# Performance work log

Hardware: AMD Instinct MI355X
Metric: run time of the kernel (lower is better)

## Reference

```python
import jax, jax.numpy as jnp
import numpy as np

N_NODES = 100000
N_EDGES = 3200000  # avg degree 32
D_IN = 256
D_OUT = 256


def setup_inputs() -> dict:
    key = jax.random.key(0)
    k1, k2, k3, k4 = jax.random.split(key, 4)
    x = jax.random.normal(k1, (N_NODES, D_IN), dtype=jnp.float32)
    # nn.Linear(in, out, bias=False): weight shape [out, in]
    W = jax.random.normal(k2, (D_OUT, D_IN), dtype=jnp.float32) / np.sqrt(D_IN).astype(np.float32)
    bias = jnp.zeros((D_OUT,), dtype=jnp.float32)
    rows = jax.random.randint(k3, (N_EDGES,), 0, N_NODES, dtype=jnp.int32)
    cols = jax.random.randint(k4, (N_EDGES,), 0, N_NODES, dtype=jnp.int32)
    return {"x": x, "W": W, "bias": bias, "rows": rows, "cols": cols}


def reference(x, W, bias, rows, cols):
    # aggr == 'planetoid-gcn-residual' branch; dropout p=0 (identity).
    n = x.shape[0]
    h = x @ W.T + bias                                      # [N, D_out]
    # adj_t.sum(dim=-1): per-row degree of binary adjacency
    deg = jax.ops.segment_sum(jnp.ones(rows.shape, x.dtype), rows, num_segments=n)
    norm = jax.lax.rsqrt(1.0 + deg)[:, None]                # [N, 1]
    h = norm * h
    # spmm_add(adj_t, h)[i] = sum_{(i,j) in E} h[j]
    agg = jax.ops.segment_sum(h[cols], rows, num_segments=n)
    h = agg + h
    return norm * h
```

## Files before the change

kernel.cpp:

```cpp
#include <hip/hip_runtime.h>
#include <hip/hip_fp16.h>
#include <stdint.h>


#define THREADS 256
#define MAXBUCK 800
#define B3_EDGES 16384

typedef _Float16 half8 __attribute__((ext_vector_type(8)));
typedef float floatx4 __attribute__((ext_vector_type(4)));

__global__ __launch_bounds__(THREADS) void bucket_count(
    const int* __restrict__ rows, int* __restrict__ bcnt, int E, int nbuck) {
    __shared__ int h[MAXBUCK];
    for (int b = threadIdx.x; b < nbuck; b += THREADS) h[b] = 0;
    __syncthreads();
    int nquad  = E >> 2;
    int stride = gridDim.x * THREADS;
    for (int q = blockIdx.x * THREADS + threadIdx.x; q < nquad; q += stride) {
        int4 r = ((const int4*)rows)[q];
        atomicAdd(&h[r.x >> 7], 1);
        atomicAdd(&h[r.y >> 7], 1);
        atomicAdd(&h[r.z >> 7], 1);
        atomicAdd(&h[r.w >> 7], 1);
    }
    if (blockIdx.x == 0)
        for (int e = (nquad << 2) + threadIdx.x; e < E; e += THREADS)
            atomicAdd(&h[rows[e] >> 7], 1);
    __syncthreads();
    for (int b = threadIdx.x; b < nbuck; b += THREADS) {
        int v = h[b];
        if (v) atomicAdd(&bcnt[b], v);
    }
}

__global__ __launch_bounds__(THREADS) void bucket_scan(
    const int* __restrict__ bcnt, int* __restrict__ boff, int* __restrict__ bcur,
    int nbuck, int E) {
    __shared__ int s[THREADS];
    int tid = threadIdx.x;
    int i0  = tid * 4;
    int v0 = (i0 + 0 < nbuck) ? bcnt[i0 + 0] : 0;
    int v1 = (i0 + 1 < nbuck) ? bcnt[i0 + 1] : 0;
    int v2 = (i0 + 2 < nbuck) ? bcnt[i0 + 2] : 0;
    int v3 = (i0 + 3 < nbuck) ? bcnt[i0 + 3] : 0;
    int sum = v0 + v1 + v2 + v3;
    s[tid] = sum;
    __syncthreads();
    for (int off = 1; off < THREADS; off <<= 1) {
        int t = (tid >= off) ? s[tid - off] : 0;
        __syncthreads();
        s[tid] += t;
        __syncthreads();
    }
    int run = s[tid] - sum;
    if (i0 + 0 < nbuck) { boff[i0 + 0] = run; bcur[i0 + 0] = run; }  run += v0;
    if (i0 + 1 < nbuck) { boff[i0 + 1] = run; bcur[i0 + 1] = run; }  run += v1;
    if (i0 + 2 < nbuck) { boff[i0 + 2] = run; bcur[i0 + 2] = run; }  run += v2;
    if (i0 + 3 < nbuck) { boff[i0 + 3] = run; bcur[i0 + 3] = run; }
    if (tid == 0) boff[nbuck] = E;
}

__global__ __launch_bounds__(THREADS) void bucket_scatter(
    const int* __restrict__ rows, const int* __restrict__ cols,
    int* __restrict__ bcur, int2* __restrict__ buf, int E, int nbuck) {
    __shared__ int h[MAXBUCK];
    __shared__ int lbase[MAXBUCK];
    for (int b = threadIdx.x; b < nbuck; b += THREADS) h[b] = 0;
    __syncthreads();
    int e0 = blockIdx.x * B3_EDGES;
    int e1 = e0 + B3_EDGES; if (e1 > E) e1 = E;
    for (int e = e0 + threadIdx.x; e < e1; e += THREADS)
        atomicAdd(&h[rows[e] >> 7], 1);
    __syncthreads();
    for (int b = threadIdx.x; b < nbuck; b += THREADS) {
        int v = h[b];
        lbase[b] = v ? atomicAdd(&bcur[b], v) : 0;
        h[b] = 0;
    }
    __syncthreads();
    for (int e = e0 + threadIdx.x; e < e1; e += THREADS) {
        int r = rows[e];
        int c = cols[e];
        int b = r >> 7;
        int p = lbase[b] + atomicAdd(&h[b], 1);
        buf[p] = make_int2(r, c);
    }
}

__global__ __launch_bounds__(THREADS) void csr_finalize(
    const int2* __restrict__ buf, const int* __restrict__ boff,
    int* __restrict__ rs, int* __restrict__ csr, int n, int E) {
    int b = blockIdx.x;
    __shared__ int h[128];
    __shared__ int base[128];
    if (threadIdx.x < 128) h[threadIdx.x] = 0;
    __syncthreads();
    int s = boff[b], e = boff[b + 1];
    for (int i = s + threadIdx.x; i < e; i += THREADS)
        atomicAdd(&h[buf[i].x & 127], 1);
    __syncthreads();
    if (threadIdx.x < 128) base[threadIdx.x] = h[threadIdx.x];
    __syncthreads();
    for (int off = 1; off < 128; off <<= 1) {
        int t = 0;
        if (threadIdx.x < 128 && threadIdx.x >= off) t = base[threadIdx.x - off];
        __syncthreads();
        if (threadIdx.x < 128) base[threadIdx.x] += t;
        __syncthreads();
    }
    if (threadIdx.x < 128) {
        int excl = s + base[threadIdx.x] - h[threadIdx.x];
        base[threadIdx.x] = excl;
        int row = (b << 7) + threadIdx.x;
        if (row < n) rs[row] = excl;
        h[threadIdx.x] = 0;
    }
    if (b == 0 && threadIdx.x == 0) rs[n] = E;
    __syncthreads();
    for (int i = s + threadIdx.x; i < e; i += THREADS) {
        int2 rc = buf[i];
        int rl = rc.x & 127;
        int p = base[rl] + atomicAdd(&h[rl], 1);
        csr[p] = rc.y;
    }
}

__global__ void make_bswz(const float* __restrict__ W, half8* __restrict__ Bswz) {
    int t = blockIdx.x * THREADS + threadIdx.x;
    int n_tile = t >> 9;
    int k_step = (t >> 6) & 7;
    int lane   = t & 63;
    int q = lane >> 4, m16 = lane & 15;
    const float* src = W + (size_t)(n_tile * 16 + m16) * 256 + k_step * 32 + q * 8;
    half8 h;
#pragma unroll
    for (int j = 0; j < 8; j++) h[j] = (_Float16)src[j];
    Bswz[t] = h;
}

__device__ __forceinline__ int As_swz(int b) {
    return b ^ ((((b >> 10) & 7) ^ (((b >> 8) & 1) << 3)) << 4);
}

__global__ __launch_bounds__(THREADS) void gemm_mfma(
    const float* __restrict__ x, const half8* __restrict__ Bswz,
    const float* __restrict__ bias, const int* __restrict__ rs,
    _Float16* __restrict__ h16, int n) {
    __shared__ _Float16 As[4 * 8 * 64 * 8];
    int tid  = threadIdx.x;
    int row0 = blockIdx.x * 64;

#pragma unroll
    for (int i = 0; i < 16; i++) {
        int flat = i * THREADS + tid;
        int r  = flat >> 6;
        int k  = (flat & 63) * 4;
        float4 v;
        if (row0 + r < n) v = *(const float4*)(x + (size_t)(row0 + r) * 256 + k);
        else { v.x = 0.f; v.y = 0.f; v.z = 0.f; v.w = 0.f; }
        int m_sub  = r >> 4;
        int k_step = k >> 5;
        int q      = (k >> 3) & 3;
        int j      = k & 7;
        int lane_w = (r & 15) + (q << 4);
        int entry  = (m_sub * 8 + k_step) * 64 + lane_w;
        union { _Float16 h[4]; uint2 u; } pk;
        pk.h[0] = (_Float16)v.x; pk.h[1] = (_Float16)v.y;
        pk.h[2] = (_Float16)v.z; pk.h[3] = (_Float16)v.w;
        *(uint2*)((char*)As + As_swz(entry * 16 + (j << 1))) = pk.u;
    }
    __syncthreads();

    int w    = tid >> 6;
    int lane = tid & 63;

    floatx4 acc[4][4];
#pragma unroll
    for (int ms = 0; ms < 4; ms++)
#pragma unroll
        for (int nn = 0; nn < 4; nn++) {
            acc[ms][nn][0] = 0.f; acc[ms][nn][1] = 0.f;
            acc[ms][nn][2] = 0.f; acc[ms][nn][3] = 0.f;
        }

    for (int ks = 0; ks < 8; ks++) {
        half8 bfrag[4];
#pragma unroll
        for (int nn = 0; nn < 4; nn++)
            bfrag[nn] = Bswz[((w * 4 + nn) * 8 + ks) * 64 + lane];
        half8 afrag[4];
#pragma unroll
        for (int ms = 0; ms < 4; ms++)
            afrag[ms] = *(const half8*)((char*)As +
                            As_swz(((ms * 8 + ks) * 64 + lane) * 16));
#pragma unroll
        for (int ms = 0; ms < 4; ms++)
#pragma unroll
            for (int nn = 0; nn < 4; nn++)
                acc[ms][nn] = __builtin_amdgcn_mfma_f32_16x16x32_f16(
                    afrag[ms], bfrag[nn], acc[ms][nn], 0, 0, 0);
    }

    int rgrp = lane >> 4;
    int cl   = lane & 15;
#pragma unroll
    for (int ms = 0; ms < 4; ms++) {
        int rbase = row0 + ms * 16 + rgrp * 4;
        float nrm[4];
#pragma unroll
        for (int i = 0; i < 4; i++) {
            int r = rbase + i;
            nrm[i] = (r < n) ? rsqrtf(1.0f + (float)(rs[r + 1] - rs[r])) : 0.f;
        }
#pragma unroll
        for (int nn = 0; nn < 4; nn++) {
            int col = w * 64 + nn * 16 + cl;
            float bb = bias[col];
#pragma unroll
            for (int i = 0; i < 4; i++) {
                int r = rbase + i;
                if (r < n)
                    h16[(size_t)r * 256 + col] =
                        (_Float16)((acc[ms][nn][i] + bb) * nrm[i]);
            }
        }
    }
}

__global__ __launch_bounds__(THREADS) void agg_half(
    const _Float16* __restrict__ h16, const int* __restrict__ csr_col,
    const int* __restrict__ rs, float* __restrict__ out, int n, int halfsel) {
    int row = blockIdx.x * 4 + (threadIdx.x >> 6);
    if (row >= n) return;
    int lane = threadIdx.x & 63;
    int g    = lane >> 4;
    int l16  = lane & 15;
    int off  = halfsel * 128 + l16 * 8;
    const _Float16* hb = h16 + off;

    int s   = rs[row];
    int end = rs[row + 1];

    float acc[8] = {0.f, 0.f, 0.f, 0.f, 0.f, 0.f, 0.f, 0.f};
    if (g == 0) {
        half8 v = *(const half8*)(hb + (size_t)row * 256);
#pragma unroll
        for (int j = 0; j < 8; j++) acc[j] = (float)v[j];
    }

    int e = s + g;
    for (; e + 4 < end; e += 8) {
        int c0 = csr_col[e];
        int c1 = csr_col[e + 4];
        half8 v0 = *(const half8*)(hb + (size_t)c0 * 256);
        half8 v1 = *(const half8*)(hb + (size_t)c1 * 256);
#pragma unroll
        for (int j = 0; j < 8; j++) acc[j] += (float)v0[j] + (float)v1[j];
    }
    for (; e < end; e += 4) {
        int c = csr_col[e];
        half8 v = *(const half8*)(hb + (size_t)c * 256);
#pragma unroll
        for (int j = 0; j < 8; j++) acc[j] += (float)v[j];
    }

#pragma unroll
    for (int j = 0; j < 8; j++) acc[j] += __shfl_down(acc[j], 32);
#pragma unroll
    for (int j = 0; j < 8; j++) acc[j] += __shfl_down(acc[j], 16);

    if (g == 0) {
        float nrm = rsqrtf(1.0f + (float)(end - s));
        float4 o0, o1;
        o0.x = acc[0] * nrm; o0.y = acc[1] * nrm; o0.z = acc[2] * nrm; o0.w = acc[3] * nrm;
        o1.x = acc[4] * nrm; o1.y = acc[5] * nrm; o1.z = acc[6] * nrm; o1.w = acc[7] * nrm;
        float* dst = out + (size_t)row * 256 + off;
        *(float4*)dst       = o0;
        *(float4*)(dst + 4) = o1;
    }
}

extern "C" void kernel_launch(void* const* d_in, const int* in_sizes, int n_in,
                              void* d_out, int out_size, void* d_ws, size_t ws_size,
                              hipStream_t stream) {
    const float* x    = (const float*)d_in[0];
    const float* W    = (const float*)d_in[1];
    const float* bias = (const float*)d_in[2];
    const int*   rows = (const int*)d_in[3];
    const int*   cols = (const int*)d_in[4];

    const int D = 256;
    int n = in_sizes[0] / D;
    int E = in_sizes[3];
    int nbuck = (n + 127) >> 7;

    char* p = (char*)d_ws;
    auto alignup = [](size_t v) { return (v + 255) & ~(size_t)255; };
    _Float16* h16 = (_Float16*)p; p += alignup((size_t)n * D * sizeof(_Float16));
    int*   rs     = (int*)p;    p += alignup((size_t)(n + 1) * sizeof(int));
    int*   csr    = (int*)p;    p += alignup((size_t)E * sizeof(int));
    half8* Bswz   = (half8*)p;  p += alignup((size_t)8192 * sizeof(half8));
    int*   bcnt   = (int*)p;    p += alignup((size_t)MAXBUCK * sizeof(int));
    int*   boff   = (int*)p;    p += alignup((size_t)(MAXBUCK + 1) * sizeof(int));
    int*   bcur   = (int*)p;    p += alignup((size_t)MAXBUCK * sizeof(int));

    int2* buf = (int2*)h16;

    hipMemsetAsync(bcnt, 0, (size_t)nbuck * sizeof(int), stream);

    bucket_count<<<256, THREADS, 0, stream>>>(rows, bcnt, E, nbuck);
    bucket_scan<<<1, THREADS, 0, stream>>>(bcnt, boff, bcur, nbuck, E);

    int b3blocks = (E + B3_EDGES - 1) / B3_EDGES;
    bucket_scatter<<<b3blocks, THREADS, 0, stream>>>(rows, cols, bcur, buf, E, nbuck);

    csr_finalize<<<nbuck, THREADS, 0, stream>>>(buf, boff, rs, csr, n, E);

    make_bswz<<<32, THREADS, 0, stream>>>(W, Bswz);

    int gblocks = (n + 63) / 64;
    gemm_mfma<<<gblocks, THREADS, 0, stream>>>(x, Bswz, bias, rs, h16, n);

    int ablocks = (n + 3) / 4;
    agg_half<<<ablocks, THREADS, 0, stream>>>(h16, csr, rs, (float*)d_out, n, 0);
    agg_half<<<ablocks, THREADS, 0, stream>>>(h16, csr, rs, (float*)d_out, n, 1);
}
```

Baseline: 570.8 us.

## Use 512-row buckets with packed 32-bit edges and LDS-staged coalesced scatter

Buckets now cover 512 rows (196 buckets) instead of 128 rows (782). Each edge is packed into one 32-bit word (local row in the high bits, column in the low 17 bits), which halves the intermediate buffer traffic. The scatter kernel sorts each edge chunk by bucket in LDS and then writes each bucket's run contiguously, so global stores are coalesced rather than scattered. The final aggregation output uses nontemporal stores. The 17-bit column packing and the 256-bucket cap limit the node count this path can handle.

After: 548.8 us. 3.9% less time.

```diff
diff --git a/kernel.cpp b/kernel.cpp
--- a/kernel.cpp
+++ b/kernel.cpp
@@ -4,34 +4,32 @@
 
 
 #define THREADS 256
-#define MAXBUCK 800
-#define B3_EDGES 16384
+#define NB 256
+#define B3_EDGES 8192
 
 typedef _Float16 half8 __attribute__((ext_vector_type(8)));
 typedef float floatx4 __attribute__((ext_vector_type(4)));
 
 __global__ __launch_bounds__(THREADS) void bucket_count(
     const int* __restrict__ rows, int* __restrict__ bcnt, int E, int nbuck) {
-    __shared__ int h[MAXBUCK];
-    for (int b = threadIdx.x; b < nbuck; b += THREADS) h[b] = 0;
+    __shared__ int h[NB];
+    h[threadIdx.x] = 0;
     __syncthreads();
     int nquad  = E >> 2;
     int stride = gridDim.x * THREADS;
     for (int q = blockIdx.x * THREADS + threadIdx.x; q < nquad; q += stride) {
         int4 r = ((const int4*)rows)[q];
-        atomicAdd(&h[r.x >> 7], 1);
-        atomicAdd(&h[r.y >> 7], 1);
-        atomicAdd(&h[r.z >> 7], 1);
-        atomicAdd(&h[r.w >> 7], 1);
+        atomicAdd(&h[r.x >> 9], 1);
+        atomicAdd(&h[r.y >> 9], 1);
+        atomicAdd(&h[r.z >> 9], 1);
+        atomicAdd(&h[r.w >> 9], 1);
     }
     if (blockIdx.x == 0)
         for (int e = (nquad << 2) + threadIdx.x; e < E; e += THREADS)
-            atomicAdd(&h[rows[e] >> 7], 1);
-    __syncthreads();
-    for (int b = threadIdx.x; b < nbuck; b += THREADS) {
-        int v = h[b];
-        if (v) atomicAdd(&bcnt[b], v);
-    }
+            atomicAdd(&h[rows[e] >> 9], 1);
+    __syncthreads();
+    int v = h[threadIdx.x];
+    if (threadIdx.x < nbuck && v) atomicAdd(&bcnt[threadIdx.x], v);
 }
 
 __global__ __launch_bounds__(THREADS) void bucket_scan(
@@ -39,13 +37,8 @@
     int nbuck, int E) {
     __shared__ int s[THREADS];
     int tid = threadIdx.x;
-    int i0  = tid * 4;
-    int v0 = (i0 + 0 < nbuck) ? bcnt[i0 + 0] : 0;
-    int v1 = (i0 + 1 < nbuck) ? bcnt[i0 + 1] : 0;
-    int v2 = (i0 + 2 < nbuck) ? bcnt[i0 + 2] : 0;
-    int v3 = (i0 + 3 < nbuck) ? bcnt[i0 + 3] : 0;
-    int sum = v0 + v1 + v2 + v3;
-    s[tid] = sum;
+    int v = (tid < nbuck) ? bcnt[tid] : 0;
+    s[tid] = v;
     __syncthreads();
     for (int off = 1; off < THREADS; off <<= 1) {
         int t = (tid >= off) ? s[tid - off] : 0;
@@ -53,76 +46,94 @@
         s[tid] += t;
         __syncthreads();
     }
-    int run = s[tid] - sum;
-    if (i0 + 0 < nbuck) { boff[i0 + 0] = run; bcur[i0 + 0] = run; }  run += v0;
-    if (i0 + 1 < nbuck) { boff[i0 + 1] = run; bcur[i0 + 1] = run; }  run += v1;
-    if (i0 + 2 < nbuck) { boff[i0 + 2] = run; bcur[i0 + 2] = run; }  run += v2;
-    if (i0 + 3 < nbuck) { boff[i0 + 3] = run; bcur[i0 + 3] = run; }
+    int excl = s[tid] - v;
+    if (tid < nbuck) { boff[tid] = excl; bcur[tid] = excl; }
     if (tid == 0) boff[nbuck] = E;
 }
 
 __global__ __launch_bounds__(THREADS) void bucket_scatter(
     const int* __restrict__ rows, const int* __restrict__ cols,
-    int* __restrict__ bcur, int2* __restrict__ buf, int E, int nbuck) {
-    __shared__ int h[MAXBUCK];
-    __shared__ int lbase[MAXBUCK];
-    for (int b = threadIdx.x; b < nbuck; b += THREADS) h[b] = 0;
+    int* __restrict__ bcur, uint32_t* __restrict__ buf, int E, int nbuck) {
+    __shared__ uint32_t staged[B3_EDGES];
+    __shared__ int h[NB], lo[NB], gb[NB], hc[NB];
+    int tid = threadIdx.x;
+    h[tid] = 0; hc[tid] = 0;
     __syncthreads();
     int e0 = blockIdx.x * B3_EDGES;
     int e1 = e0 + B3_EDGES; if (e1 > E) e1 = E;
-    for (int e = e0 + threadIdx.x; e < e1; e += THREADS)
-        atomicAdd(&h[rows[e] >> 7], 1);
-    __syncthreads();
-    for (int b = threadIdx.x; b < nbuck; b += THREADS) {
-        int v = h[b];
-        lbase[b] = v ? atomicAdd(&bcur[b], v) : 0;
-        h[b] = 0;
-    }
-    __syncthreads();
-    for (int e = e0 + threadIdx.x; e < e1; e += THREADS) {
+    for (int e = e0 + tid; e < e1; e += THREADS)
+        atomicAdd(&h[rows[e] >> 9], 1);
+    __syncthreads();
+    int v = h[tid];
+    lo[tid] = v;
+    __syncthreads();
+    for (int off = 1; off < NB; off <<= 1) {
+        int t = (tid >= off) ? lo[tid - off] : 0;
+        __syncthreads();
+        lo[tid] += t;
+        __syncthreads();
+    }
+    int excl = lo[tid] - v;
+    __syncthreads();
+    lo[tid] = excl;
+    gb[tid] = (tid < nbuck && v) ? atomicAdd(&bcur[tid], v) : 0;
+    __syncthreads();
+    for (int e = e0 + tid; e < e1; e += THREADS) {
         int r = rows[e];
         int c = cols[e];
-        int b = r >> 7;
-        int p = lbase[b] + atomicAdd(&h[b], 1);
-        buf[p] = make_int2(r, c);
+        int b = r >> 9;
+        int p = lo[b] + atomicAdd(&hc[b], 1);
+        staged[p] = ((uint32_t)(r & 511) << 17) | (uint32_t)c;
+    }
+    __syncthreads();
+    int wid = tid >> 6, lane = tid & 63;
+    for (int b = wid; b < nbuck; b += 4) {
+        int cnt = h[b], src = lo[b], dst = gb[b];
+        for (int i = lane; i < cnt; i += 64)
+            buf[dst + i] = staged[src + i];
     }
 }
 
 __global__ __launch_bounds__(THREADS) void csr_finalize(
-    const int2* __restrict__ buf, const int* __restrict__ boff,
+    const uint32_t* __restrict__ buf, const int* __restrict__ boff,
     int* __restrict__ rs, int* __restrict__ csr, int n, int E) {
-    int b = blockIdx.x;
-    __shared__ int h[128];
-    __shared__ int base[128];
-    if (threadIdx.x < 128) h[threadIdx.x] = 0;
+    int b   = blockIdx.x;
+    int tid = threadIdx.x;
+    __shared__ int h[512], base[512], s1[THREADS];
+    h[tid] = 0; h[tid + 256] = 0;
     __syncthreads();
     int s = boff[b], e = boff[b + 1];
-    for (int i = s + threadIdx.x; i < e; i += THREADS)
-        atomicAdd(&h[buf[i].x & 127], 1);
-    __syncthreads();
-    if (threadIdx.x < 128) base[threadIdx.x] = h[threadIdx.x];
-    __syncthreads();
-    for (int off = 1; off < 128; off <<= 1) {
-        int t = 0;
-        if (threadIdx.x < 128 && threadIdx.x >= off) t = base[threadIdx.x - off];
-        __syncthreads();
-        if (threadIdx.x < 128) base[threadIdx.x] += t;
-        __syncthreads();
-    }
-    if (threadIdx.x < 128) {
-        int excl = s + base[threadIdx.x] - h[threadIdx.x];
-        base[threadIdx.x] = excl;
-        int row = (b << 7) + threadIdx.x;
-        if (row < n) rs[row] = excl;
-        h[threadIdx.x] = 0;
-    }
-    if (b == 0 && threadIdx.x == 0) rs[n] = E;
-    __syncthreads();
-    for (int i = s + threadIdx.x; i < e; i += THREADS) {
-        int2 rc = buf[i];
-        int rl = rc.x & 127;
-        int p = base[rl] + atomicAdd(&h[rl], 1);
-        csr[p] = rc.y;
+    for (int i = s + tid; i < e; i += THREADS)
+        atomicAdd(&h[buf[i] >> 17], 1);
+    __syncthreads();
+    int a0 = h[2 * tid], a1 = h[2 * tid + 1];
+    s1[tid] = a0 + a1;
+    __syncthreads();
+    for (int off = 1; off < THREADS; off <<= 1) {
+        int t = (tid >= off) ? s1[tid - off] : 0;
+        __syncthreads();
+        s1[tid] += t;
+        __syncthreads();
+    }
+    int eps = s1[tid] - (a0 + a1);
+    base[2 * tid]     = s + eps;
+    base[2 * tid + 1] = s + eps + a0;
+    __syncthreads();
+#pragma unroll
+    for (int j = 0; j < 2; j++) {
+        int rl  = tid + j * 256;
+        int row = (b << 9) + rl;
+        if (row < n) rs[row] = base[rl];
+        h[rl] = 0;
+    }
+    if (b == 0 && tid == 0) rs[n] = E;
+    __syncthreads();
+    for (int i = s + tid; i < e; i += THREADS) {
+        uint32_t v = buf[i];
+        int rl = v >> 17;
+        int c  = v & 0x1FFFF;
+        int p  = base[rl] + atomicAdd(&h[rl], 1);
+        csr[p] = c;
     }
 }
 
@@ -272,12 +283,12 @@
 
     if (g == 0) {
         float nrm = rsqrtf(1.0f + (float)(end - s));
-        float4 o0, o1;
-        o0.x = acc[0] * nrm; o0.y = acc[1] * nrm; o0.z = acc[2] * nrm; o0.w = acc[3] * nrm;
-        o1.x = acc[4] * nrm; o1.y = acc[5] * nrm; o1.z = acc[6] * nrm; o1.w = acc[7] * nrm;
+        floatx4 o0, o1;
+        o0[0] = acc[0] * nrm; o0[1] = acc[1] * nrm; o0[2] = acc[2] * nrm; o0[3] = acc[3] * nrm;
+        o1[0] = acc[4] * nrm; o1[1] = acc[5] * nrm; o1[2] = acc[6] * nrm; o1[3] = acc[7] * nrm;
         float* dst = out + (size_t)row * 256 + off;
-        *(float4*)dst       = o0;
-        *(float4*)(dst + 4) = o1;
+        __builtin_nontemporal_store(o0, (floatx4*)dst);
+        __builtin_nontemporal_store(o1, (floatx4*)(dst + 4));
     }
 }
 
@@ -293,7 +304,7 @@
     const int D = 256;
     int n = in_sizes[0] / D;
     int E = in_sizes[3];
-    int nbuck = (n + 127) >> 7;
+    int nbuck = (n + 511) >> 9;
 
     char* p = (char*)d_ws;
     auto alignup = [](size_t v) { return (v + 255) & ~(size_t)255; };
@@ -301,11 +312,11 @@
     int*   rs     = (int*)p;    p += alignup((size_t)(n + 1) * sizeof(int));
     int*   csr    = (int*)p;    p += alignup((size_t)E * sizeof(int));
     half8* Bswz   = (half8*)p;  p += alignup((size_t)8192 * sizeof(half8));
-    int*   bcnt   = (int*)p;    p += alignup((size_t)MAXBUCK * sizeof(int));
-    int*   boff   = (int*)p;    p += alignup((size_t)(MAXBUCK + 1) * sizeof(int));
-    int*   bcur   = (int*)p;    p += alignup((size_t)MAXBUCK * sizeof(int));
-
-    int2* buf = (int2*)h16;
+    int*   bcnt   = (int*)p;    p += alignup((size_t)NB * sizeof(int));
+    int*   boff   = (int*)p;    p += alignup((size_t)(NB + 1) * sizeof(int));
+    int*   bcur   = (int*)p;    p += alignup((size_t)NB * sizeof(int));
+
+    uint32_t* buf = (uint32_t*)h16;
 
     hipMemsetAsync(bcnt, 0, (size_t)nbuck * sizeof(int), stream);
 
```
